# Kernel tuning notes

Hardware: AMD Instinct MI355X
Metric: run time of the kernel (lower is better)

Reference implementation:

```python
import jax, jax.numpy as jnp
import numpy as np

B, N, DEG = 128, 512, 8          # graphs, nodes per graph, avg degree
E = B * N * DEG                  # 524288 edges
F_IN, H1, H2, C = 128, 64, 128, 10
RATIO = 0.8
K = int(np.ceil(RATIO * N))      # TopKPooling keeps ceil(0.8*N)=410 nodes per graph


def setup_inputs() -> dict:
    key = jax.random.key(0)
    ks = jax.random.split(key, 10)
    n_nodes = B * N
    x = jax.random.normal(ks[0], (n_nodes, F_IN), dtype=jnp.float32)
    # random intra-graph edges, then offset node ids per graph
    src = jax.random.randint(ks[1], (B, N * DEG), 0, N)
    dst = jax.random.randint(ks[2], (B, N * DEG), 0, N)
    off = (jnp.arange(B) * N)[:, None]
    edge_index = jnp.stack([(src + off).reshape(-1), (dst + off).reshape(-1)]).astype(jnp.int64)
    batch = jnp.repeat(jnp.arange(B), N).astype(jnp.int64)
    s1 = 1.0 / np.sqrt(F_IN)
    s2 = 1.0 / np.sqrt(H1)
    s3 = 1.0 / np.sqrt(H2)
    return {
        "x": x,
        "edge_index": edge_index,
        "batch": batch,
        "W1": jax.random.uniform(ks[3], (F_IN, H1), jnp.float32, -s1, s1),
        "b1": jnp.zeros((H1,), jnp.float32),
        "W2": jax.random.uniform(ks[4], (H1, H2), jnp.float32, -s2, s2),
        "b2": jnp.zeros((H2,), jnp.float32),
        "pool_w": jax.random.uniform(ks[5], (H2,), jnp.float32, -s3, s3),
        "fc_W": jax.random.uniform(ks[6], (H2, C), jnp.float32, -s3, s3),
        "fc_b": jax.random.uniform(ks[7], (C,), jnp.float32, -s3, s3),
    }


def gcn_conv(x, W, b, src, dst, num_nodes):
    # PyG GCNConv: add self-loops, symmetric normalization, scatter-add aggregation
    loop = jnp.arange(num_nodes)
    src = jnp.concatenate([src, loop])
    dst = jnp.concatenate([dst, loop])
    deg = jax.ops.segment_sum(jnp.ones_like(src, dtype=x.dtype), dst, num_segments=num_nodes)
    dis = jnp.where(deg > 0, jax.lax.rsqrt(jnp.maximum(deg, 1.0)), 0.0)
    norm = dis[src] * dis[dst]                       # [E+N]
    h = x @ W                                        # transform first (smaller of the two in conv1)
    out = jax.ops.segment_sum(norm[:, None] * h[src], dst, num_segments=num_nodes)
    return out + b


def reference(x, edge_index, batch, W1, b1, W2, b2, pool_w, fc_W, fc_b):
    num_nodes = x.shape[0]
    src, dst = edge_index[0], edge_index[1]
    x = jax.nn.relu(gcn_conv(x, W1, b1, src, dst, num_nodes))
    x = jax.nn.relu(gcn_conv(x, W2, b2, src, dst, num_nodes))
    # TopKPooling: score = (x . w)/||w||, per-graph top-k on raw score, gate by tanh(score)
    score = (x @ pool_w) / jnp.linalg.norm(pool_w)   # [B*N]
    score_b = score.reshape(B, N)
    top_vals, top_idx = jax.lax.top_k(score_b, K)    # [B, K]
    x_b = x.reshape(B, N, H2)
    x_sel = jnp.take_along_axis(x_b, top_idx[:, :, None], axis=1)   # [B, K, H2]
    x_sel = x_sel * jnp.tanh(top_vals)[:, :, None]
    # global max pool over each (pooled) graph; pooled edge_index is unused downstream
    g = jnp.max(x_sel, axis=1)                        # [B, H2]
    logits = g @ fc_W + fc_b                          # [B, C]
    return jax.nn.log_softmax(logits, axis=1)
```

## Files before the change

### kernel.cpp

```cpp
#include <hip/hip_runtime.h>
#include <hip/hip_bf16.h>


#define BB 128
#define NN 512
#define NODES (BB*NN)
#define EE (BB*NN*8)
#define EDGPG (NN*8)
#define F_IN 128
#define H1 64
#define H2 128
#define NC 10
#define KSEL 410
#define ROWCAP 48

typedef unsigned short u16;
typedef unsigned int   u32;

static __device__ __forceinline__ float lo2f(u32 u){ return __uint_as_float(u << 16); }
static __device__ __forceinline__ float hi2f(u32 u){ return __uint_as_float(u & 0xffff0000u); }
static __device__ __forceinline__ u16 f2b(float f){
    __hip_bfloat16 h = __float2bfloat16(f);
    return *reinterpret_cast<u16*>(&h);
}
static __device__ __forceinline__ u32 packbf(float a, float b){
    return (u32)f2b(a) | ((u32)f2b(b) << 16);
}
static __device__ __forceinline__ void acc8s(float* a, uint4 v, float ds){
    a[0] = fmaf(ds, lo2f(v.x), a[0]); a[1] = fmaf(ds, hi2f(v.x), a[1]);
    a[2] = fmaf(ds, lo2f(v.y), a[2]); a[3] = fmaf(ds, hi2f(v.y), a[3]);
    a[4] = fmaf(ds, lo2f(v.z), a[4]); a[5] = fmaf(ds, hi2f(v.z), a[5]);
    a[6] = fmaf(ds, lo2f(v.w), a[6]); a[7] = fmaf(ds, hi2f(v.w), a[7]);
}
static __device__ __forceinline__ void acc8(float* a, uint4 v){
    a[0] += lo2f(v.x); a[1] += hi2f(v.x);
    a[2] += lo2f(v.y); a[3] += hi2f(v.y);
    a[4] += lo2f(v.z); a[5] += hi2f(v.z);
    a[6] += lo2f(v.w); a[7] += hi2f(v.w);
}
static __device__ __forceinline__ int swz2048(int bid){
    return ((bid & 7) << 8) | (bid >> 3);
}
static __device__ __forceinline__ int swz1024(int bid){
    return ((bid & 7) << 7) | (bid >> 3);
}

static __device__ __forceinline__ bool ei_is_i64(const int* __restrict__ ei){
    return ((ei[1] | ei[3] | ei[5] | ei[7]) == 0);
}
static __device__ __forceinline__ int ld_src(const int* __restrict__ ei, int e, bool w64){
    return w64 ? ei[2*e] : ei[e];
}
static __device__ __forceinline__ int ld_dst(const int* __restrict__ ei, int e, bool w64){
    return w64 ? ei[2*(EE + e)] : ei[EE + e];
}

#define G1NODES 128
#define XPAD 68
__global__ __launch_bounds__(256) void k_prep_gemm1(const int* __restrict__ ei,
                                                    const float* __restrict__ x,
                                                    const float* __restrict__ W1,
                                                    int* __restrict__ cnt,
                                                    int* __restrict__ adj,
                                                    u32* __restrict__ h1u){
    __shared__ __align__(16) float Ws[64*H1];
    __shared__ __align__(16) float xs[G1NODES*XPAD];
    bool w64 = ei_is_i64(ei);
    int t = threadIdx.x;
    int gb = (int)blockIdx.x;
    int b  = gb >> 2;
    int sub = gb & 3;
    int node0 = b*NN + sub*G1NODES;

    #pragma unroll
    for (int i = 0; i < 4; ++i){
        int e = b*EDGPG + sub*1024 + i*256 + t;
        int d = (ld_dst(ei, e, w64) - b*NN) & (NN - 1);
        int s = ld_src(ei, e, w64) & (NODES - 1);
        int node = b*NN + d;
        int p = atomicAdd(&cnt[node], 1);
        if (p < ROWCAP - 1) adj[node*ROWCAP + 1 + p] = s;
    }
    if (t < G1NODES){
        int node = node0 + t;
        adj[node*ROWCAP] = node;
    }

    int tc = t & 7, tr = t >> 3;
    int j0 = tc*8;
    float acc[4][8] = {};
    for (int half = 0; half < 2; ++half){
        const float4* Wv = (const float4*)(W1 + half*4096);
        for (int i = t; i < 1024; i += 256)
            *(float4*)&Ws[i*4] = Wv[i];
        for (int i = t; i < 2048; i += 256){
            int node = i >> 4, c = i & 15;
            float4 v = *(const float4*)(x + (size_t)(node0 + node)*F_IN + half*64 + c*4);
            *(float4*)&xs[node*XPAD + c*4] = v;
        }
        __syncthreads();
        #pragma unroll 2
        for (int k = 0; k < 64; k += 4){
            float4 xv0 = *(const float4*)&xs[(tr +  0)*XPAD + k];
            float4 xv1 = *(const float4*)&xs[(tr + 32)*XPAD + k];
            float4 xv2 = *(const float4*)&xs[(tr + 64)*XPAD + k];
            float4 xv3 = *(const float4*)&xs[(tr + 96)*XPAD + k];
            float xa0[4] = {xv0.x, xv0.y, xv0.z, xv0.w};
            float xa1[4] = {xv1.x, xv1.y, xv1.z, xv1.w};
            float xa2[4] = {xv2.x, xv2.y, xv2.z, xv2.w};
            float xa3[4] = {xv3.x, xv3.y, xv3.z, xv3.w};
            #pragma unroll
            for (int kk = 0; kk < 4; ++kk){
                float4 wa = *(const float4*)&Ws[(k+kk)*H1 + j0];
                float4 wb = *(const float4*)&Ws[(k+kk)*H1 + j0 + 4];
                acc[0][0] += xa0[kk]*wa.x; acc[0][1] += xa0[kk]*wa.y; acc[0][2] += xa0[kk]*wa.z; acc[0][3] += xa0[kk]*wa.w;
                acc[0][4] += xa0[kk]*wb.x; acc[0][5] += xa0[kk]*wb.y; acc[0][6] += xa0[kk]*wb.z; acc[0][7] += xa0[kk]*wb.w;
                acc[1][0] += xa1[kk]*wa.x; acc[1][1] += xa1[kk]*wa.y; acc[1][2] += xa1[kk]*wa.z; acc[1][3] += xa1[kk]*wa.w;
                acc[1][4] += xa1[kk]*wb.x; acc[1][5] += xa1[kk]*wb.y; acc[1][6] += xa1[kk]*wb.z; acc[1][7] += xa1[kk]*wb.w;
                acc[2][0] += xa2[kk]*wa.x; acc[2][1] += xa2[kk]*wa.y; acc[2][2] += xa2[kk]*wa.z; acc[2][3] += xa2[kk]*wa.w;
                acc[2][4] += xa2[kk]*wb.x; acc[2][5] += xa2[kk]*wb.y; acc[2][6] += xa2[kk]*wb.z; acc[2][7] += xa2[kk]*wb.w;
                acc[3][0] += xa3[kk]*wa.x; acc[3][1] += xa3[kk]*wa.y; acc[3][2] += xa3[kk]*wa.z; acc[3][3] += xa3[kk]*wa.w;
                acc[3][4] += xa3[kk]*wb.x; acc[3][5] += xa3[kk]*wb.y; acc[3][6] += xa3[kk]*wb.z; acc[3][7] += xa3[kk]*wb.w;
            }
        }
        __syncthreads();
    }
    #pragma unroll
    for (int i = 0; i < 4; ++i){
        int node = node0 + tr + 32*i;
        *(uint4*)&h1u[(size_t)node*32 + tc*4] =
            make_uint4(packbf(acc[i][0], acc[i][1]), packbf(acc[i][2], acc[i][3]),
                       packbf(acc[i][4], acc[i][5]), packbf(acc[i][6], acc[i][7]));
    }
}

__global__ __launch_bounds__(256) void k_agg1(const uint4* __restrict__ h1v,
                                              const int* __restrict__ cnt,
                                              const int* __restrict__ adj,
                                              const float4* __restrict__ b1v,
                                              uint4* __restrict__ a1v){
    __shared__ float disl[NN];
    int t = threadIdx.x;
    int lb = swz2048((int)blockIdx.x);
    int node0 = lb*32;
    int gbase = node0 & ~(NN - 1);
    for (int i = t; i < NN; i += 256){
        int c = cnt[gbase + i]; if (c > ROWCAP-1) c = ROWCAP-1;
        disl[i] = rsqrtf((float)(c + 1));
    }
    __syncthreads();
    int node = node0 + (t >> 3);
    int fl = t & 7;
    int rs = node*ROWCAP;
    int c = cnt[node]; if (c > ROWCAP-1) c = ROWCAP-1;
    int pe = rs + c + 1;
    float a0[8] = {}, a1r[8] = {}, a2r[8] = {}, a3r[8] = {};
    int p = rs;
    for (; p + 4 <= pe; p += 4){
        int s0 = adj[p], s1 = adj[p+1], s2 = adj[p+2], s3 = adj[p+3];
        float d0 = disl[s0 & (NN-1)], d1 = disl[s1 & (NN-1)];
        float d2 = disl[s2 & (NN-1)], d3 = disl[s3 & (NN-1)];
        uint4 v0 = h1v[s0*8 + fl];
        uint4 v1 = h1v[s1*8 + fl];
        uint4 v2 = h1v[s2*8 + fl];
        uint4 v3 = h1v[s3*8 + fl];
        acc8s(a0, v0, d0); acc8s(a1r, v1, d1); acc8s(a2r, v2, d2); acc8s(a3r, v3, d3);
    }
    for (; p < pe; ++p){
        int s = adj[p];
        acc8s(a0, h1v[s*8 + fl], disl[s & (NN-1)]);
    }
    float r[8];
    #pragma unroll
    for (int j = 0; j < 8; ++j) r[j] = (a0[j] + a1r[j]) + (a2r[j] + a3r[j]);
    float dn = disl[node & (NN-1)];
    float4 bA = b1v[2*fl], bB = b1v[2*fl+1];
    float w0 = dn*r[0] + bA.x; w0 = w0 > 0.f ? w0 : 0.f;
    float w1 = dn*r[1] + bA.y; w1 = w1 > 0.f ? w1 : 0.f;
    float w2 = dn*r[2] + bA.z; w2 = w2 > 0.f ? w2 : 0.f;
    float w3 = dn*r[3] + bA.w; w3 = w3 > 0.f ? w3 : 0.f;
    float w4 = dn*r[4] + bB.x; w4 = w4 > 0.f ? w4 : 0.f;
    float w5 = dn*r[5] + bB.y; w5 = w5 > 0.f ? w5 : 0.f;
    float w6 = dn*r[6] + bB.z; w6 = w6 > 0.f ? w6 : 0.f;
    float w7 = dn*r[7] + bB.w; w7 = w7 > 0.f ? w7 : 0.f;
    a1v[node*8 + fl] = make_uint4(packbf(dn*w0, dn*w1), packbf(dn*w2, dn*w3),
                                  packbf(dn*w4, dn*w5), packbf(dn*w6, dn*w7));
}

#define G2NODES 64
#define APAD 68
__global__ __launch_bounds__(256) void k_gemm2s(const uint4* __restrict__ a1v,
                                                const int* __restrict__ cnt,
                                                const int* __restrict__ adj,
                                                const float* __restrict__ W2,
                                                const float* __restrict__ b2,
                                                const float* __restrict__ pw,
                                                u32* __restrict__ a2u,
                                                float* __restrict__ score){
    __shared__ __align__(16) float Ws[32*H2];
    __shared__ __align__(16) float as[G2NODES*APAD];
    __shared__ float pws[H2];
    int t = threadIdx.x;
    int lb = swz1024((int)blockIdx.x);
    int node0 = lb*G2NODES;
    if (t < H2) pws[t] = pw[t];
    {
        int fl = t & 7, ng = t >> 3;
        for (int pass = 0; pass < 2; ++pass){
            int nl = ng + pass*32;
            int node = node0 + nl;
            int rs = node*ROWCAP;
            int c = cnt[node]; if (c > ROWCAP-1) c = ROWCAP-1;
            int pe = rs + c + 1;
            float a0[8] = {}, a1r[8] = {}, a2r[8] = {}, a3r[8] = {};
            int p = rs;
            for (; p + 4 <= pe; p += 4){
                int s0 = adj[p], s1 = adj[p+1], s2 = adj[p+2], s3 = adj[p+3];
                uint4 v0 = a1v[s0*8 + fl];
                uint4 v1 = a1v[s1*8 + fl];
                uint4 v2 = a1v[s2*8 + fl];
                uint4 v3 = a1v[s3*8 + fl];
                acc8(a0, v0); acc8(a1r, v1); acc8(a2r, v2); acc8(a3r, v3);
            }
            for (; p < pe; ++p){
                uint4 v = a1v[adj[p]*8 + fl];
                acc8(a0, v);
            }
            float dn = rsqrtf((float)(c + 1));
            float* dst = &as[nl*APAD + 8*fl];
            float r0 = dn*((a0[0] + a1r[0]) + (a2r[0] + a3r[0]));
            float r1 = dn*((a0[1] + a1r[1]) + (a2r[1] + a3r[1]));
            float r2 = dn*((a0[2] + a1r[2]) + (a2r[2] + a3r[2]));
            float r3 = dn*((a0[3] + a1r[3]) + (a2r[3] + a3r[3]));
            float r4 = dn*((a0[4] + a1r[4]) + (a2r[4] + a3r[4]));
            float r5 = dn*((a0[5] + a1r[5]) + (a2r[5] + a3r[5]));
            float r6 = dn*((a0[6] + a1r[6]) + (a2r[6] + a3r[6]));
            float r7 = dn*((a0[7] + a1r[7]) + (a2r[7] + a3r[7]));
            *(float4*)&dst[0] = make_float4(r0, r1, r2, r3);
            *(float4*)&dst[4] = make_float4(r4, r5, r6, r7);
        }
    }
    int tc = t & 15, tr = t >> 4;
    int j0 = tc*8;
    float acc[4][8] = {};
    for (int half = 0; half < 2; ++half){
        const float4* Wv = (const float4*)(W2 + half*4096);
        for (int i = t; i < 1024; i += 256)
            *(float4*)&Ws[i*4] = Wv[i];
        __syncthreads();
        int kb = half*32;
        #pragma unroll 2
        for (int k = 0; k < 32; k += 4){
            float4 xv0 = *(const float4*)&as[(tr +  0)*APAD + kb + k];
            float4 xv1 = *(const float4*)&as[(tr + 16)*APAD + kb + k];
            float4 xv2 = *(const float4*)&as[(tr + 32)*APAD + kb + k];
            float4 xv3 = *(const float4*)&as[(tr + 48)*APAD + kb + k];
            float xa0[4] = {xv0.x, xv0.y, xv0.z, xv0.w};
            float xa1[4] = {xv1.x, xv1.y, xv1.z, xv1.w};
            float xa2[4] = {xv2.x, xv2.y, xv2.z, xv2.w};
            float xa3[4] = {xv3.x, xv3.y, xv3.z, xv3.w};
            #pragma unroll
            for (int kk = 0; kk < 4; ++kk){
                float4 wa = *(const float4*)&Ws[(k+kk)*H2 + j0];
                float4 wb = *(const float4*)&Ws[(k+kk)*H2 + j0 + 4];
                acc[0][0] += xa0[kk]*wa.x; acc[0][1] += xa0[kk]*wa.y; acc[0][2] += xa0[kk]*wa.z; acc[0][3] += xa0[kk]*wa.w;
                acc[0][4] += xa0[kk]*wb.x; acc[0][5] += xa0[kk]*wb.y; acc[0][6] += xa0[kk]*wb.z; acc[0][7] += xa0[kk]*wb.w;
                acc[1][0] += xa1[kk]*wa.x; acc[1][1] += xa1[kk]*wa.y; acc[1][2] += xa1[kk]*wa.z; acc[1][3] += xa1[kk]*wa.w;
                acc[1][4] += xa1[kk]*wb.x; acc[1][5] += xa1[kk]*wb.y; acc[1][6] += xa1[kk]*wb.z; acc[1][7] += xa1[kk]*wb.w;
                acc[2][0] += xa2[kk]*wa.x; acc[2][1] += xa2[kk]*wa.y; acc[2][2] += xa2[kk]*wa.z; acc[2][3] += xa2[kk]*wa.w;
                acc[2][4] += xa2[kk]*wb.x; acc[2][5] += xa2[kk]*wb.y; acc[2][6] += xa2[kk]*wb.z; acc[2][7] += xa2[kk]*wb.w;
                acc[3][0] += xa3[kk]*wa.x; acc[3][1] += xa3[kk]*wa.y; acc[3][2] += xa3[kk]*wa.z; acc[3][3] += xa3[kk]*wa.w;
                acc[3][4] += xa3[kk]*wb.x; acc[3][5] += xa3[kk]*wb.y; acc[3][6] += xa3[kk]*wb.z; acc[3][7] += xa3[kk]*wb.w;
            }
        }
        __syncthreads();
    }
    float p0 = pws[j0],   p1 = pws[j0+1], p2 = pws[j0+2], p3 = pws[j0+3];
    float p4 = pws[j0+4], p5 = pws[j0+5], p6 = pws[j0+6], p7 = pws[j0+7];
    float bj[8];
    #pragma unroll
    for (int c2 = 0; c2 < 8; ++c2) bj[c2] = b2[j0 + c2];
    #pragma unroll
    for (int i = 0; i < 4; ++i){
        int node = node0 + tr + 16*i;
        float v0 = acc[i][0] + bj[0]; v0 = v0 > 0.f ? v0 : 0.f;
        float v1 = acc[i][1] + bj[1]; v1 = v1 > 0.f ? v1 : 0.f;
        float v2 = acc[i][2] + bj[2]; v2 = v2 > 0.f ? v2 : 0.f;
        float v3 = acc[i][3] + bj[3]; v3 = v3 > 0.f ? v3 : 0.f;
        float v4 = acc[i][4] + bj[4]; v4 = v4 > 0.f ? v4 : 0.f;
        float v5 = acc[i][5] + bj[5]; v5 = v5 > 0.f ? v5 : 0.f;
        float v6 = acc[i][6] + bj[6]; v6 = v6 > 0.f ? v6 : 0.f;
        float v7 = acc[i][7] + bj[7]; v7 = v7 > 0.f ? v7 : 0.f;
        *(uint4*)&a2u[(size_t)node*64 + tc*4] =
            make_uint4(packbf(v0, v1), packbf(v2, v3), packbf(v4, v5), packbf(v6, v7));
        float sp = v0*p0 + v1*p1 + v2*p2 + v3*p3 + v4*p4 + v5*p5 + v6*p6 + v7*p7;
        sp += __shfl_xor(sp, 8, 16);
        sp += __shfl_xor(sp, 4, 16);
        sp += __shfl_xor(sp, 2, 16);
        sp += __shfl_xor(sp, 1, 16);
        if (tc == 0) score[node] = sp;
    }
}

__global__ __launch_bounds__(512) void k_pool(const u32* __restrict__ a2u,
                                              const float* __restrict__ score,
                                              const float* __restrict__ pw,
                                              const float* __restrict__ fcW,
                                              const float* __restrict__ fcb,
                                              float* __restrict__ out){
    __shared__ float so[NN];
    __shared__ float ss[NN];
    __shared__ float th[NN];
    __shared__ float pm[32*H2];
    __shared__ float gl[H2];
    __shared__ float fws[H2*NC];
    __shared__ float lg[NC];
    __shared__ float red[3];
    int b = blockIdx.x, t = threadIdx.x;
    for (int i = t; i < H2*NC; i += 512) fws[i] = fcW[i];
    if (t < H2){ float v = pw[t]; gl[t] = v*v; }
    __syncthreads();
    if (t == 0){
        float s = 0.f;
        for (int i = 0; i < H2; ++i) s += gl[i];
        red[2] = rsqrtf(s);
    }
    __syncthreads();
    float pwinv = red[2];
    float sc = score[b*NN + t];
    so[t] = sc; ss[t] = sc; th[t] = tanhf(sc*pwinv);
    __syncthreads();
    for (int k = 2; k <= NN; k <<= 1){
        for (int j = k >> 1; j > 0; j >>= 1){
            int ixj = t ^ j;
            if (ixj > t){
                float a = ss[t], c = ss[ixj];
                bool desc = ((t & k) == 0);
                bool sw = desc ? (a < c) : (a > c);
                if (sw){ ss[t] = c; ss[ixj] = a; }
            }
            __syncthreads();
        }
    }
    float thresh = ss[KSEL-1];
    float mask_t = (so[t] >= thresh) ? 0.f : -INFINITY;
    __syncthreads();
    so[t] = mask_t;
    __syncthreads();
    int tc = t & 15, q = t >> 4;
    const uint4* ap = (const uint4*)(a2u + (size_t)b*NN*64);
    float m0 = -INFINITY, m1 = -INFINITY, m2 = -INFINITY, m3 = -INFINITY;
    float m4 = -INFINITY, m5 = -INFINITY, m6 = -INFINITY, m7 = -INFINITY;
    int nb = q*16;
    #pragma unroll 4
    for (int n = nb; n < nb + 16; ++n){
        uint4 v = ap[(size_t)n*16 + tc];
        float thn = th[n], son = so[n];
        m0 = fmaxf(m0, lo2f(v.x)*thn + son);
        m1 = fmaxf(m1, hi2f(v.x)*thn + son);
        m2 = fmaxf(m2, lo2f(v.y)*thn + son);
        m3 = fmaxf(m3, hi2f(v.y)*thn + son);
        m4 = fmaxf(m4, lo2f(v.z)*thn + son);
        m5 = fmaxf(m5, hi2f(v.z)*thn + son);
        m6 = fmaxf(m6, lo2f(v.w)*thn + son);
        m7 = fmaxf(m7, hi2f(v.w)*thn + son);
    }
    float* pmr = &pm[q*H2 + 8*tc];
    pmr[0] = m0; pmr[1] = m1; pmr[2] = m2; pmr[3] = m3;
    pmr[4] = m4; pmr[5] = m5; pmr[6] = m6; pmr[7] = m7;
    __syncthreads();
    if (t < H2){
        float g = pm[t];
        #pragma unroll
        for (int qq = 1; qq < 32; ++qq) g = fmaxf(g, pm[qq*H2 + t]);
        gl[t] = g;
    }
    __syncthreads();
    if (t < NC){
        float acc = fcb[t];
        for (int k2 = 0; k2 < H2; ++k2) acc += gl[k2]*fws[k2*NC + t];
        lg[t] = acc;
    }
    __syncthreads();
    if (t == 0){
        float mx = lg[0];
        for (int i = 1; i < NC; ++i) mx = fmaxf(mx, lg[i]);
        float s = 0.f;
        for (int i = 0; i < NC; ++i) s += expf(lg[i] - mx);
        red[0] = mx; red[1] = logf(s);
    }
    __syncthreads();
    if (t < NC) out[b*NC + t] = lg[t] - red[0] - red[1];
}

extern "C" void kernel_launch(void* const* d_in, const int* in_sizes, int n_in,
                              void* d_out, int out_size, void* d_ws, size_t ws_size,
                              hipStream_t stream) {
    const float* x   = (const float*)d_in[0];
    const int*   ei  = (const int*)d_in[1];
    const float* W1  = (const float*)d_in[3];
    const float* b1  = (const float*)d_in[4];
    const float* W2  = (const float*)d_in[5];
    const float* b2  = (const float*)d_in[6];
    const float* pw  = (const float*)d_in[7];
    const float* fcW = (const float*)d_in[8];
    const float* fcb = (const float*)d_in[9];

    char* ws = (char*)d_ws;
    int*   cnt   = (int*)(ws + 4096);
    float* score = (float*)(ws + 524288);
    int*   adj   = (int*)(ws + 4194304);
    u32*   h1u   = (u32*)(ws + 16777216);
    u32*   a1u   = (u32*)(ws + 25165824);
    u32*   a2u   = (u32*)(ws + 33554432);

    hipMemsetAsync(cnt, 0, NODES*sizeof(int), stream);
    k_prep_gemm1<<<NODES/G1NODES, 256, 0, stream>>>(ei, x, W1, cnt, adj, h1u);
    k_agg1<<<NODES/32, 256, 0, stream>>>((const uint4*)h1u, cnt, adj,
                                         (const float4*)b1, (uint4*)a1u);
    k_gemm2s<<<NODES/G2NODES, 256, 0, stream>>>((const uint4*)a1u, cnt, adj,
                                                W2, b2, pw, a2u, score);
    k_pool<<<BB, 512, 0, stream>>>(a2u, score, pw, fcW, fcb, (float*)d_out);
}
```

Before: 176.4 us.

## Split adjacency build from GEMM1, retile GEMM1, use register bitonic sort in pool

Splits the fused edge-bucketing and first-layer GEMM into a separate k_build kernel (one thread per edge) and a standalone k_gemm1 with smaller 64-node tiles, 512 threads and 2x4 outputs per thread. The aim is more parallelism and shorter critical paths per block than the fused kernel had. The pooling kernel's bitonic sort now keeps values in registers, using warp shuffles for strides below 64 and shared memory only for larger strides, which cuts the per-step shared-memory traffic and barriers. Costs are an extra kernel launch and lower register reuse per thread in the GEMM (narrower stores).

```diff
diff --git a/kernel.cpp b/kernel.cpp
--- a/kernel.cpp
+++ b/kernel.cpp
@@ -55,45 +55,41 @@
     return w64 ? ei[2*(EE + e)] : ei[EE + e];
 }
 
-#define G1NODES 128
+__global__ __launch_bounds__(512) void k_build(const int* __restrict__ ei,
+                                               int* __restrict__ cnt,
+                                               int* __restrict__ adj){
+    bool w64 = ei_is_i64(ei);
+    int t = threadIdx.x;
+    int e = (int)blockIdx.x*512 + t;
+    int b = e >> 12;
+    int d = (ld_dst(ei, e, w64) - b*NN) & (NN - 1);
+    int s = ld_src(ei, e, w64) & (NODES - 1);
+    int node = b*NN + d;
+    int p = atomicAdd(&cnt[node], 1);
+    if (p < ROWCAP - 1) adj[node*ROWCAP + 1 + p] = s;
+    if (blockIdx.x < BB){
+        int sn = (int)blockIdx.x*NN + t;
+        adj[sn*ROWCAP] = sn;
+    }
+}
+
+#define G1NODES 64
 #define XPAD 68
-__global__ __launch_bounds__(256) void k_prep_gemm1(const int* __restrict__ ei,
-                                                    const float* __restrict__ x,
-                                                    const float* __restrict__ W1,
-                                                    int* __restrict__ cnt,
-                                                    int* __restrict__ adj,
-                                                    u32* __restrict__ h1u){
+__global__ __launch_bounds__(512) void k_gemm1(const float* __restrict__ x,
+                                               const float* __restrict__ W1,
+                                               u32* __restrict__ h1u){
     __shared__ __align__(16) float Ws[64*H1];
     __shared__ __align__(16) float xs[G1NODES*XPAD];
-    bool w64 = ei_is_i64(ei);
     int t = threadIdx.x;
-    int gb = (int)blockIdx.x;
-    int b  = gb >> 2;
-    int sub = gb & 3;
-    int node0 = b*NN + sub*G1NODES;
-
-    #pragma unroll
-    for (int i = 0; i < 4; ++i){
-        int e = b*EDGPG + sub*1024 + i*256 + t;
-        int d = (ld_dst(ei, e, w64) - b*NN) & (NN - 1);
-        int s = ld_src(ei, e, w64) & (NODES - 1);
-        int node = b*NN + d;
-        int p = atomicAdd(&cnt[node], 1);
-        if (p < ROWCAP - 1) adj[node*ROWCAP + 1 + p] = s;
-    }
-    if (t < G1NODES){
-        int node = node0 + t;
-        adj[node*ROWCAP] = node;
-    }
-
-    int tc = t & 7, tr = t >> 3;
-    int j0 = tc*8;
-    float acc[4][8] = {};
+    int node0 = (int)blockIdx.x*G1NODES;
+    int tc = t & 15, tr = t >> 4;
+    int j0 = tc*4, n0 = tr*2;
+    float acc[2][4] = {};
     for (int half = 0; half < 2; ++half){
         const float4* Wv = (const float4*)(W1 + half*4096);
-        for (int i = t; i < 1024; i += 256)
+        for (int i = t; i < 1024; i += 512)
             *(float4*)&Ws[i*4] = Wv[i];
-        for (int i = t; i < 2048; i += 256){
+        for (int i = t; i < 1024; i += 512){
             int node = i >> 4, c = i & 15;
             float4 v = *(const float4*)(x + (size_t)(node0 + node)*F_IN + half*64 + c*4);
             *(float4*)&xs[node*XPAD + c*4] = v;
@@ -101,36 +97,25 @@
         __syncthreads();
         #pragma unroll 2
         for (int k = 0; k < 64; k += 4){
-            float4 xv0 = *(const float4*)&xs[(tr +  0)*XPAD + k];
-            float4 xv1 = *(const float4*)&xs[(tr + 32)*XPAD + k];
-            float4 xv2 = *(const float4*)&xs[(tr + 64)*XPAD + k];
-            float4 xv3 = *(const float4*)&xs[(tr + 96)*XPAD + k];
+            float4 xv0 = *(const float4*)&xs[(n0+0)*XPAD + k];
+            float4 xv1 = *(const float4*)&xs[(n0+1)*XPAD + k];
             float xa0[4] = {xv0.x, xv0.y, xv0.z, xv0.w};
             float xa1[4] = {xv1.x, xv1.y, xv1.z, xv1.w};
-            float xa2[4] = {xv2.x, xv2.y, xv2.z, xv2.w};
-            float xa3[4] = {xv3.x, xv3.y, xv3.z, xv3.w};
             #pragma unroll
             for (int kk = 0; kk < 4; ++kk){
-                float4 wa = *(const float4*)&Ws[(k+kk)*H1 + j0];
-                float4 wb = *(const float4*)&Ws[(k+kk)*H1 + j0 + 4];
-                acc[0][0] += xa0[kk]*wa.x; acc[0][1] += xa0[kk]*wa.y; acc[0][2] += xa0[kk]*wa.z; acc[0][3] += xa0[kk]*wa.w;
-                acc[0][4] += xa0[kk]*wb.x; acc[0][5] += xa0[kk]*wb.y; acc[0][6] += xa0[kk]*wb.z; acc[0][7] += xa0[kk]*wb.w;
-                acc[1][0] += xa1[kk]*wa.x; acc[1][1] += xa1[kk]*wa.y; acc[1][2] += xa1[kk]*wa.z; acc[1][3] += xa1[kk]*wa.w;
-                acc[1][4] += xa1[kk]*wb.x; acc[1][5] += xa1[kk]*wb.y; acc[1][6] += xa1[kk]*wb.z; acc[1][7] += xa1[kk]*wb.w;
-                acc[2][0] += xa2[kk]*wa.x; acc[2][1] += xa2[kk]*wa.y; acc[2][2] += xa2[kk]*wa.z; acc[2][3] += xa2[kk]*wa.w;
-                acc[2][4] += xa2[kk]*wb.x; acc[2][5] += xa2[kk]*wb.y; acc[2][6] += xa2[kk]*wb.z; acc[2][7] += xa2[kk]*wb.w;
-                acc[3][0] += xa3[kk]*wa.x; acc[3][1] += xa3[kk]*wa.y; acc[3][2] += xa3[kk]*wa.z; acc[3][3] += xa3[kk]*wa.w;
-                acc[3][4] += xa3[kk]*wb.x; acc[3][5] += xa3[kk]*wb.y; acc[3][6] += xa3[kk]*wb.z; acc[3][7] += xa3[kk]*wb.w;
+                float4 wv = *(const float4*)&Ws[(k+kk)*H1 + j0];
+                acc[0][0] += xa0[kk]*wv.x; acc[0][1] += xa0[kk]*wv.y; acc[0][2] += xa0[kk]*wv.z; acc[0][3] += xa0[kk]*wv.w;
+                acc[1][0] += xa1[kk]*wv.x; acc[1][1] += xa1[kk]*wv.y; acc[1][2] += xa1[kk]*wv.z; acc[1][3] += xa1[kk]*wv.w;
             }
         }
         __syncthreads();
     }
     #pragma unroll
-    for (int i = 0; i < 4; ++i){
-        int node = node0 + tr + 32*i;
-        *(uint4*)&h1u[(size_t)node*32 + tc*4] =
-            make_uint4(packbf(acc[i][0], acc[i][1]), packbf(acc[i][2], acc[i][3]),
-                       packbf(acc[i][4], acc[i][5]), packbf(acc[i][6], acc[i][7]));
+    for (int i = 0; i < 2; ++i){
+        int node = node0 + n0 + i;
+        size_t base = (size_t)node*32 + tc*2;
+        h1u[base]     = packbf(acc[i][0], acc[i][1]);
+        h1u[base + 1] = packbf(acc[i][2], acc[i][3]);
     }
 }
 
@@ -328,20 +313,26 @@
     __syncthreads();
     float pwinv = red[2];
     float sc = score[b*NN + t];
-    so[t] = sc; ss[t] = sc; th[t] = tanhf(sc*pwinv);
-    __syncthreads();
+    so[t] = sc; th[t] = tanhf(sc*pwinv);
+    float v = sc;
     for (int k = 2; k <= NN; k <<= 1){
         for (int j = k >> 1; j > 0; j >>= 1){
-            int ixj = t ^ j;
-            if (ixj > t){
-                float a = ss[t], c = ss[ixj];
-                bool desc = ((t & k) == 0);
-                bool sw = desc ? (a < c) : (a > c);
-                if (sw){ ss[t] = c; ss[ixj] = a; }
+            bool desc  = ((t & k) == 0);
+            bool lower = ((t & j) == 0);
+            bool wantmax = (desc == lower);
+            float c;
+            if (j >= 64){
+                ss[t] = v; __syncthreads();
+                c = ss[t ^ j];
+                __syncthreads();
+            } else {
+                c = __shfl_xor(v, j, 64);
             }
-            __syncthreads();
+            v = wantmax ? fmaxf(v, c) : fminf(v, c);
         }
     }
+    ss[t] = v;
+    __syncthreads();
     float thresh = ss[KSEL-1];
     float mask_t = (so[t] >= thresh) ? 0.f : -INFINITY;
     __syncthreads();
@@ -354,16 +345,16 @@
     int nb = q*16;
     #pragma unroll 4
     for (int n = nb; n < nb + 16; ++n){
-        uint4 v = ap[(size_t)n*16 + tc];
+        uint4 vv = ap[(size_t)n*16 + tc];
         float thn = th[n], son = so[n];
-        m0 = fmaxf(m0, lo2f(v.x)*thn + son);
-        m1 = fmaxf(m1, hi2f(v.x)*thn + son);
-        m2 = fmaxf(m2, lo2f(v.y)*thn + son);
-        m3 = fmaxf(m3, hi2f(v.y)*thn + son);
-        m4 = fmaxf(m4, lo2f(v.z)*thn + son);
-        m5 = fmaxf(m5, hi2f(v.z)*thn + son);
-        m6 = fmaxf(m6, lo2f(v.w)*thn + son);
-        m7 = fmaxf(m7, hi2f(v.w)*thn + son);
+        m0 = fmaxf(m0, lo2f(vv.x)*thn + son);
+        m1 = fmaxf(m1, hi2f(vv.x)*thn + son);
+        m2 = fmaxf(m2, lo2f(vv.y)*thn + son);
+        m3 = fmaxf(m3, hi2f(vv.y)*thn + son);
+        m4 = fmaxf(m4, lo2f(vv.z)*thn + son);
+        m5 = fmaxf(m5, hi2f(vv.z)*thn + son);
+        m6 = fmaxf(m6, lo2f(vv.w)*thn + son);
+        m7 = fmaxf(m7, hi2f(vv.w)*thn + son);
     }
     float* pmr = &pm[q*H2 + 8*tc];
     pmr[0] = m0; pmr[1] = m1; pmr[2] = m2; pmr[3] = m3;
@@ -415,7 +406,8 @@
     u32*   a2u   = (u32*)(ws + 33554432);
 
     hipMemsetAsync(cnt, 0, NODES*sizeof(int), stream);
-    k_prep_gemm1<<<NODES/G1NODES, 256, 0, stream>>>(ei, x, W1, cnt, adj, h1u);
+    k_build<<<EE/512, 512, 0, stream>>>(ei, cnt, adj);
+    k_gemm1<<<NODES/G1NODES, 512, 0, stream>>>(x, W1, h1u);
     k_agg1<<<NODES/32, 256, 0, stream>>>((const uint4*)h1u, cnt, adj,
                                          (const float4*)b1, (uint4*)a1u);
     k_gemm2s<<<NODES/G2NODES, 256, 0, stream>>>((const uint4*)a1u, cnt, adj,
```

Result: slower. 181.5 us (+2.9%).
